# Performance work log

Measured on AMD Instinct MI355X. Metric: run time of the kernel, lower is better.

The kernel has to match this reference:

```python
import jax, jax.numpy as jnp
import numpy as np

B, S, D, E, K = 4, 2048, 1024, 8, 2


def setup_inputs() -> dict:
    key = jax.random.key(0)
    k1, k2, k3 = jax.random.split(key, 3)
    scale = 1.0 / np.sqrt(D)
    x = jax.random.normal(k1, (B, S, D), dtype=jnp.float32)
    Wg = jax.random.normal(k2, (D, E), dtype=jnp.float32) * scale
    bg = jnp.zeros((E,), dtype=jnp.float32)
    We = jax.random.normal(k3, (E, D, D), dtype=jnp.float32) * scale
    be = jnp.zeros((E, D), dtype=jnp.float32)
    return {"x": x, "Wg": Wg, "bg": bg, "We": We, "be": be}


def reference(x, Wg, bg, We, be):
    # gate scores: [B, S, E]
    gate_scores = jnp.einsum("bsd,de->bse", x, Wg) + bg
    topk_values, topk_indices = jax.lax.top_k(gate_scores, K)
    # mask: -inf everywhere except at top-k indices (where value == score)
    sel = jax.nn.one_hot(topk_indices, E, dtype=jnp.bool_).any(axis=-2)  # [B,S,E]
    masked = jnp.where(sel, gate_scores, -jnp.inf)
    gate_weights = jax.nn.softmax(masked, axis=-1)  # [B,S,E]
    # dense all-expert compute, as in the original: [B,S,E,D]
    expert_outputs = jnp.einsum("bsd,edh->bseh", x, We) + be
    fused = jnp.einsum("bse,bseh->bsh", gate_weights, expert_outputs)
    return fused
```

## Files before the change

### kernel.cpp

```cpp
#include <hip/hip_runtime.h>
#include <stdint.h>

#define NTOK   8192
#define DIM    1024
#define NEXP   8
#define MAXP   8192

typedef float    f32x4  __attribute__((ext_vector_type(4)));
typedef __bf16   bf16x8 __attribute__((ext_vector_type(8)));
typedef _Float16 h16x8  __attribute__((ext_vector_type(8)));

typedef __attribute__((address_space(1))) const void* gas_ptr;
typedef __attribute__((address_space(3))) void*       las_ptr;

__device__ __forceinline__ unsigned short f32_to_bf16(float f) {
  union { float f; unsigned int u; } v; v.f = f;
  unsigned int u = v.u;
  unsigned int r = (u + 0x7FFFu + ((u >> 16) & 1u)) >> 16;
  return (unsigned short)r;
}

__global__ __launch_bounds__(256) void wprep_kernel(
    const float* __restrict__ We, unsigned short* __restrict__ Wf) {
  __shared__ float tile[64][65];
  const int bid = blockIdx.x;
  const int e  = bid >> 8;
  const int d0 = ((bid >> 4) & 15) * 64;
  const int h0 = (bid & 15) * 64;
  const int t  = threadIdx.x;
  const float* src = We + (size_t)e * DIM * DIM;
  const int rr = t >> 4;
  const int cc = (t & 15) * 4;
#pragma unroll
  for (int p = 0; p < 4; ++p) {
    const int row = rr + p * 16;
    f32x4 v = *(const f32x4*)(src + (size_t)(d0 + row) * DIM + (h0 + cc));
    tile[row][cc]     = v[0];
    tile[row][cc + 1] = v[1];
    tile[row][cc + 2] = v[2];
    tile[row][cc + 3] = v[3];
  }
  __syncthreads();
  const int nt    = h0 >> 7;
  const int rbase = h0 & 64;
  const int hl    = t >> 2;
  const int k8    = t & 3;
#pragma unroll
  for (int reg = 0; reg < 2; ++reg) {
    const int kt = (d0 >> 5) + reg;
    unsigned int pk[4];
#pragma unroll
    for (int q = 0; q < 4; ++q) {
      int dl = reg * 32 + k8 * 8 + q * 2;
      pk[q] = (unsigned int)f32_to_bf16(tile[dl][hl]) |
              ((unsigned int)f32_to_bf16(tile[dl + 1][hl]) << 16);
    }
    size_t base = (((size_t)(e * 8 + nt) * 32 + kt) << 12) +
                  (size_t)(rbase + hl) * 32 + k8 * 8;
    *(uint4*)&Wf[base] = make_uint4(pk[0], pk[1], pk[2], pk[3]);
  }
}

__global__ __launch_bounds__(256) void gate_kernel(
    const float* __restrict__ x, const float* __restrict__ Wg,
    const float* __restrict__ bg, unsigned short* __restrict__ Xbf,
    int* __restrict__ tok_ee, float2* __restrict__ tok_w) {
  const int wave = threadIdx.x >> 6;
  const int lane = threadIdx.x & 63;
  const int tok0 = blockIdx.x * 16 + wave * 4;

  float xs[4][16];
#pragma unroll
  for (int t = 0; t < 4; ++t) {
    const float* xr = x + (size_t)(tok0 + t) * DIM + lane * 16;
#pragma unroll
    for (int i = 0; i < 4; ++i)
      *(f32x4*)&xs[t][i * 4] = *(const f32x4*)(xr + i * 4);
  }
#pragma unroll
  for (int t = 0; t < 4; ++t) {
    unsigned int pk[8];
#pragma unroll
    for (int i = 0; i < 8; ++i)
      pk[i] = (unsigned int)f32_to_bf16(xs[t][2 * i]) |
              ((unsigned int)f32_to_bf16(xs[t][2 * i + 1]) << 16);
    uint4* xb = (uint4*)(Xbf + (size_t)(tok0 + t) * DIM + lane * 16);
    xb[0] = make_uint4(pk[0], pk[1], pk[2], pk[3]);
    xb[1] = make_uint4(pk[4], pk[5], pk[6], pk[7]);
  }

  double acc[4][8];
#pragma unroll
  for (int t = 0; t < 4; ++t)
#pragma unroll
    for (int e = 0; e < 8; ++e) acc[t][e] = 0.0;

  const float* wr = Wg + (size_t)(lane * 16) * NEXP;
#pragma unroll
  for (int i = 0; i < 16; ++i) {
    f32x4 wa = *(const f32x4*)(wr + i * 8);
    f32x4 wb = *(const f32x4*)(wr + i * 8 + 4);
    double w0 = wa[0], w1 = wa[1], w2 = wa[2], w3 = wa[3];
    double w4 = wb[0], w5 = wb[1], w6 = wb[2], w7 = wb[3];
#pragma unroll
    for (int t = 0; t < 4; ++t) {
      double xd = (double)xs[t][i];
      acc[t][0] += xd * w0; acc[t][1] += xd * w1;
      acc[t][2] += xd * w2; acc[t][3] += xd * w3;
      acc[t][4] += xd * w4; acc[t][5] += xd * w5;
      acc[t][6] += xd * w6; acc[t][7] += xd * w7;
    }
  }
#pragma unroll
  for (int m = 1; m < 64; m <<= 1)
#pragma unroll
    for (int t = 0; t < 4; ++t)
#pragma unroll
      for (int e = 0; e < 8; ++e) acc[t][e] += __shfl_xor(acc[t][e], m, 64);

  if (lane == 0) {
#pragma unroll
    for (int t = 0; t < 4; ++t) {
      float s[8];
#pragma unroll
      for (int e = 0; e < 8; ++e) s[e] = (float)acc[t][e] + bg[e];
      int i0 = 0; float v0 = s[0];
#pragma unroll
      for (int e = 1; e < 8; ++e) if (s[e] > v0) { v0 = s[e]; i0 = e; }
      int i1 = -1; float v1 = -3.4e38f;
#pragma unroll
      for (int e = 0; e < 8; ++e) if (e != i0 && s[e] > v1) { v1 = s[e]; i1 = e; }
      float t1 = expf(v1 - v0);
      float den = 1.0f + t1;
      tok_ee[tok0 + t] = i0 | (i1 << 8);
      tok_w[tok0 + t]  = make_float2(1.0f / den, t1 / den);
    }
  }
}

__global__ __launch_bounds__(1024) void compact_kernel(
    const int* __restrict__ tok_ee, const float2* __restrict__ tok_w,
    int* __restrict__ counts, int* __restrict__ pair_token,
    float* __restrict__ pair_w) {
  __shared__ int wave_cnt[16];
  __shared__ int wave_off[16];
  const int e = blockIdx.x;
  const int tid = threadIdx.x, wave = tid >> 6, lane = tid & 63;
  int base = 0;
  for (int c = 0; c < NTOK / 1024; ++c) {
    const int t = c * 1024 + tid;
    const int p = tok_ee[t];
    const bool m0 = ((p & 255) == e);
    const bool m1 = (((p >> 8) & 255) == e);
    const unsigned long long m = __ballot(m0 || m1);
    const int pre = __popcll(m & ((1ull << lane) - 1ull));
    if (lane == 0) wave_cnt[wave] = __popcll(m);
    __syncthreads();
    if (tid == 0) {
      int s = base;
      for (int w = 0; w < 16; ++w) { wave_off[w] = s; s += wave_cnt[w]; }
      base = s;
    }
    __syncthreads();
    if (m0 || m1) {
      const float2 w = tok_w[t];
      const int slot = wave_off[wave] + pre;
      pair_token[e * MAXP + slot] = (t << 1) | (m1 ? 1 : 0);
      pair_w[e * MAXP + slot]     = m1 ? w.y : w.x;
    }
    __syncthreads();
  }
  if (tid == 0) counts[e] = base;
}

__global__ __launch_bounds__(512, 4) void moe_gemm(
    const unsigned short* __restrict__ Xbf, const unsigned short* __restrict__ Wf,
    const float* __restrict__ be, const int* __restrict__ counts,
    const int* __restrict__ pair_token, const float* __restrict__ pair_w,
    _Float16* __restrict__ part, float* __restrict__ Y, int use_part) {
  const int id    = blockIdx.x;
  const int e     = id & 7;
  const int ntile = (id >> 3) & 3;
  const int m0    = (id >> 5) * 128;
  const int cnt   = counts[e];
  if (m0 >= cnt) return;

  __shared__ __align__(16) unsigned short As[3][128 * 32];
  __shared__ __align__(16) unsigned short Bs[3][256 * 32];

  const int tid  = threadIdx.x;
  const int wave = tid >> 6;
  const int lane = tid & 63;
  const int fm   = lane & 15;
  const int fq   = lane >> 4;
  const int wm   = wave >> 2;
  const int wn   = wave & 3;

  const int kc = (((lane & 3) ^ ((lane >> 3) & 3)) * 8);
  const int grA = m0 + wave * 16 + (lane >> 2);
  const int tkA = (grA < cnt) ? (pair_token[e * MAXP + grA] >> 1) : 0;
  const unsigned short* gA = Xbf + (size_t)tkA * DIM + kc;
  const unsigned short* gB[2];
#pragma unroll
  for (int l = 0; l < 2; ++l) {
    const int R16 = wave * 2 + l;
    const int cg  = ntile * 2 + (R16 >> 3);
    gB[l] = Wf + ((size_t)(e * 8 + cg) << 17) +
            (size_t)((R16 & 7) * 16 + (lane >> 2)) * 32 + kc;
  }

#define STAGE(buf, k0v)                                                       \
  {                                                                           \
    __builtin_amdgcn_global_load_lds(                                         \
        (gas_ptr)(uintptr_t)(gA + (k0v)),                                     \
        (las_ptr)(uintptr_t)(&As[buf][wave * 512]), 16, 0, 0);                \
    _Pragma("unroll") for (int l = 0; l < 2; ++l)                             \
      __builtin_amdgcn_global_load_lds(                                       \
          (gas_ptr)(uintptr_t)(gB[l] + (size_t)(k0v) * 128),                  \
          (las_ptr)(uintptr_t)(&Bs[buf][(wave * 2 + l) * 512]), 16, 0, 0);    \
  }

  f32x4 acc[4][4];
#pragma unroll
  for (int i = 0; i < 4; ++i)
#pragma unroll
    for (int j = 0; j < 4; ++j) { f32x4 z = {0.f, 0.f, 0.f, 0.f}; acc[i][j] = z; }

  const int rdo  = (fq ^ ((fm >> 1) & 3)) * 8;
  const int arow = (wm * 64 + fm) * 32 + rdo;
  const int brow = (wn * 64 + fm) * 32 + rdo;

  STAGE(0, 0);
  STAGE(1, 32);
  int cur = 0;
  for (int k0 = 0; k0 < DIM; k0 += 32) {
    asm volatile("s_waitcnt vmcnt(3)" ::: "memory");
    __builtin_amdgcn_s_barrier();

    int kn = k0 + 64;
    if (kn >= DIM) kn = 0;
    int nb = cur + 2;
    if (nb >= 3) nb -= 3;
    STAGE(nb, kn);

    bf16x8 af[4], bfr[4];
#pragma unroll
    for (int i = 0; i < 4; ++i)
      af[i] = *(const bf16x8*)&As[cur][arow + i * 512];
#pragma unroll
    for (int j = 0; j < 4; ++j)
      bfr[j] = *(const bf16x8*)&Bs[cur][brow + j * 512];
#pragma unroll
    for (int i = 0; i < 4; ++i)
#pragma unroll
      for (int j = 0; j < 4; ++j)
        acc[i][j] = __builtin_amdgcn_mfma_f32_16x16x32_bf16(af[i], bfr[j],
                                                            acc[i][j], 0, 0, 0);
    cur = (cur + 1 == 3) ? 0 : cur + 1;
  }
  asm volatile("s_waitcnt vmcnt(0)" ::: "memory");
#undef STAGE

#pragma unroll
  for (int i = 0; i < 4; ++i) {
    int   rv[4];
    float wv[4];
#pragma unroll
    for (int r = 0; r < 4; ++r) {
      int gr = m0 + wm * 64 + i * 16 + fq * 4 + r;
      bool valid = gr < cnt;
      rv[r] = valid ? pair_token[e * MAXP + gr] : -1;
      wv[r] = valid ? pair_w[e * MAXP + gr] : 0.f;
    }
    if (use_part) {
#pragma unroll
      for (int j = 0; j < 4; ++j) {
        int col = ntile * 256 + wn * 64 + j * 16 + fm;
        float bev = be[e * DIM + col];
#pragma unroll
        for (int r = 0; r < 4; ++r) {
          int v = rv[r];
          if (v >= 0)
            __builtin_nontemporal_store(
                (_Float16)(wv[r] * (acc[i][j][r] + bev)),
                &part[(size_t)v * DIM + col]);
        }
      }
    } else {
#pragma unroll
      for (int j = 0; j < 4; ++j) {
        int col = ntile * 256 + wn * 64 + j * 16 + fm;
        float bev = be[e * DIM + col];
#pragma unroll
        for (int r = 0; r < 4; ++r) {
          int v = rv[r];
          if (v >= 0)
            atomicAdd(Y + (size_t)(v >> 1) * DIM + col,
                      wv[r] * (acc[i][j][r] + bev));
        }
      }
    }
  }
}

__global__ __launch_bounds__(256) void reduce_pairs(
    const _Float16* __restrict__ part, float* __restrict__ Y) {
  const int g = blockIdx.x * 256 + threadIdx.x;
  const int t = g >> 7;
  const int o = (g & 127) * 8;
  const h16x8 a =
      __builtin_nontemporal_load((const h16x8*)(part + (size_t)(2 * t) * DIM + o));
  const h16x8 b =
      __builtin_nontemporal_load((const h16x8*)(part + (size_t)(2 * t + 1) * DIM + o));
  float* y = Y + (size_t)t * DIM + o;
  f32x4 lo = {(float)a[0] + (float)b[0], (float)a[1] + (float)b[1],
              (float)a[2] + (float)b[2], (float)a[3] + (float)b[3]};
  f32x4 hi = {(float)a[4] + (float)b[4], (float)a[5] + (float)b[5],
              (float)a[6] + (float)b[6], (float)a[7] + (float)b[7]};
  __builtin_nontemporal_store(lo, (f32x4*)y);
  __builtin_nontemporal_store(hi, (f32x4*)(y + 4));
}

extern "C" void kernel_launch(void* const* d_in, const int* in_sizes, int n_in,
                              void* d_out, int out_size, void* d_ws, size_t ws_size,
                              hipStream_t stream) {
  const float* x  = (const float*)d_in[0];
  const float* Wg = (const float*)d_in[1];
  const float* bg = (const float*)d_in[2];
  const float* We = (const float*)d_in[3];
  const float* be = (const float*)d_in[4];
  float* Y = (float*)d_out;

  const size_t MB = 1024 * 1024;
  char* ws = (char*)d_ws;
  unsigned short* Xbf = (unsigned short*)ws;
  unsigned short* Wf  = (unsigned short*)(ws + 16 * MB);
  const size_t part_bytes = (size_t)NTOK * 2 * DIM * 2;
  const size_t need = 32 * MB + part_bytes + 1 * MB;
  const int use_part = ws_size >= need;
  _Float16* part = (_Float16*)(ws + 32 * MB);
  char* p2 = ws + 32 * MB + (use_part ? part_bytes : 0);
  int*    counts     = (int*)p2;
  int*    pair_token = (int*)(p2 + 256);
  float*  pair_w     = (float*)(p2 + 256 + 262144);
  int*    tok_ee     = (int*)(p2 + 256 + 2 * 262144);
  float2* tok_w      = (float2*)(p2 + 256 + 2 * 262144 + 32768);

  if (!use_part)
    hipMemsetAsync(d_out, 0, (size_t)out_size * sizeof(float), stream);

  wprep_kernel<<<2048, 256, 0, stream>>>(We, Wf);
  gate_kernel<<<512, 256, 0, stream>>>(x, Wg, bg, Xbf, tok_ee, tok_w);
  compact_kernel<<<NEXP, 1024, 0, stream>>>(tok_ee, tok_w, counts, pair_token,
                                            pair_w);
  moe_gemm<<<8 * 4 * (MAXP / 128), 512, 0, stream>>>(
      Xbf, Wf, be, counts, pair_token, pair_w, part, Y, use_part);
  if (use_part)
    reduce_pairs<<<NTOK * DIM / 8 / 256, 256, 0, stream>>>(part, Y);
}
```

Before: 219.2 us.

## Pre-gather routed token rows into tiled contiguous A buffer before MoE GEMM

Adds a gather kernel that copies each expert's routed bf16 token rows into a k-tiled, contiguous layout (Ap) matching the GEMM's LDS tile format. The GEMM then streams A tiles with contiguous loads instead of indirect per-row gathers from Xbf, for the first 4096 slots per expert. This removes scattered row reads from the GEMM's inner loop but adds an extra kernel launch and a 64 MB write plus re-read of workspace. The new path only runs if the workspace is large enough.

```diff
diff --git a/kernel.cpp b/kernel.cpp
--- a/kernel.cpp
+++ b/kernel.cpp
@@ -6,9 +6,10 @@
 #define NEXP   8
 #define MAXP   8192
 
-typedef float    f32x4  __attribute__((ext_vector_type(4)));
-typedef __bf16   bf16x8 __attribute__((ext_vector_type(8)));
-typedef _Float16 h16x8  __attribute__((ext_vector_type(8)));
+typedef float        f32x4  __attribute__((ext_vector_type(4)));
+typedef unsigned int u32x4  __attribute__((ext_vector_type(4)));
+typedef __bf16       bf16x8 __attribute__((ext_vector_type(8)));
+typedef _Float16     h16x8  __attribute__((ext_vector_type(8)));
 
 typedef __attribute__((address_space(1))) const void* gas_ptr;
 typedef __attribute__((address_space(3))) void*       las_ptr;
@@ -57,7 +58,8 @@
     }
     size_t base = (((size_t)(e * 8 + nt) * 32 + kt) << 12) +
                   (size_t)(rbase + hl) * 32 + k8 * 8;
-    *(uint4*)&Wf[base] = make_uint4(pk[0], pk[1], pk[2], pk[3]);
+    u32x4 w = {pk[0], pk[1], pk[2], pk[3]};
+    *(u32x4*)&Wf[base] = w;
   }
 }
 
@@ -84,9 +86,11 @@
     for (int i = 0; i < 8; ++i)
       pk[i] = (unsigned int)f32_to_bf16(xs[t][2 * i]) |
               ((unsigned int)f32_to_bf16(xs[t][2 * i + 1]) << 16);
-    uint4* xb = (uint4*)(Xbf + (size_t)(tok0 + t) * DIM + lane * 16);
-    xb[0] = make_uint4(pk[0], pk[1], pk[2], pk[3]);
-    xb[1] = make_uint4(pk[4], pk[5], pk[6], pk[7]);
+    u32x4* xb = (u32x4*)(Xbf + (size_t)(tok0 + t) * DIM + lane * 16);
+    u32x4 w0 = {pk[0], pk[1], pk[2], pk[3]};
+    u32x4 w1 = {pk[4], pk[5], pk[6], pk[7]};
+    xb[0] = w0;
+    xb[1] = w1;
   }
 
   double acc[4][8];
@@ -173,11 +177,51 @@
   if (tid == 0) counts[e] = base;
 }
 
+__global__ __launch_bounds__(256) void gather_kernel(
+    const unsigned short* __restrict__ Xbf, const int* __restrict__ counts,
+    const int* __restrict__ pair_token, unsigned short* __restrict__ Ap) {
+  __shared__ __align__(16) unsigned short rows[16][1040];
+  const int bid = blockIdx.x;
+  const int e  = bid & 7;
+  const int g  = (bid >> 3) & 7;
+  const int mt = bid >> 6;
+  const int cnt = counts[e];
+  const int m0g = mt * 128 + g * 16;
+  if (m0g >= ((cnt + 127) & ~127)) return;
+  const int wave = threadIdx.x >> 6, lane = threadIdx.x & 63;
+#pragma unroll
+  for (int q = 0; q < 4; ++q) {
+    const int r    = wave * 4 + q;
+    const int slot = m0g + r;
+    u32x4 v0 = {0u, 0u, 0u, 0u}, v1 = {0u, 0u, 0u, 0u};
+    if (slot < cnt) {
+      const int tok = pair_token[e * MAXP + slot] >> 1;
+      const u32x4* src = (const u32x4*)(Xbf + (size_t)tok * DIM + lane * 8);
+      v0 = src[0];
+      v1 = src[64];
+    }
+    *(u32x4*)&rows[r][lane * 8]       = v0;
+    *(u32x4*)&rows[r][lane * 8 + 512] = v1;
+  }
+  __syncthreads();
+  const int r  = lane >> 2;
+  const int k8 = lane & 3;
+  unsigned short* dst0 = Ap + (((size_t)(e * 32 + mt) * 32) << 12) +
+                         (size_t)(g * 16 + r) * 32 + k8 * 8;
+#pragma unroll
+  for (int q = 0; q < 8; ++q) {
+    const int kt = wave * 8 + q;
+    u32x4 v = *(const u32x4*)&rows[r][kt * 32 + k8 * 8];
+    __builtin_nontemporal_store(v, (u32x4*)(dst0 + ((size_t)kt << 12)));
+  }
+}
+
 __global__ __launch_bounds__(512, 4) void moe_gemm(
     const unsigned short* __restrict__ Xbf, const unsigned short* __restrict__ Wf,
-    const float* __restrict__ be, const int* __restrict__ counts,
-    const int* __restrict__ pair_token, const float* __restrict__ pair_w,
-    _Float16* __restrict__ part, float* __restrict__ Y, int use_part) {
+    const unsigned short* __restrict__ Ap, const float* __restrict__ be,
+    const int* __restrict__ counts, const int* __restrict__ pair_token,
+    const float* __restrict__ pair_w, _Float16* __restrict__ part,
+    float* __restrict__ Y, int use_part, int use_ap) {
   const int id    = blockIdx.x;
   const int e     = id & 7;
   const int ntile = (id >> 3) & 3;
@@ -197,9 +241,18 @@
   const int wn   = wave & 3;
 
   const int kc = (((lane & 3) ^ ((lane >> 3) & 3)) * 8);
-  const int grA = m0 + wave * 16 + (lane >> 2);
-  const int tkA = (grA < cnt) ? (pair_token[e * MAXP + grA] >> 1) : 0;
-  const unsigned short* gA = Xbf + (size_t)tkA * DIM + kc;
+  const unsigned short* gA;
+  size_t astep;
+  if (use_ap && m0 < 4096) {
+    gA = Ap + (((size_t)(e * 32 + (m0 >> 7)) * 32) << 12) +
+         (size_t)(wave * 16 + (lane >> 2)) * 32 + kc;
+    astep = 128;
+  } else {
+    const int grA = m0 + wave * 16 + (lane >> 2);
+    const int tkA = (grA < cnt) ? (pair_token[e * MAXP + grA] >> 1) : 0;
+    gA = Xbf + (size_t)tkA * DIM + kc;
+    astep = 1;
+  }
   const unsigned short* gB[2];
 #pragma unroll
   for (int l = 0; l < 2; ++l) {
@@ -212,7 +265,7 @@
 #define STAGE(buf, k0v)                                                       \
   {                                                                           \
     __builtin_amdgcn_global_load_lds(                                         \
-        (gas_ptr)(uintptr_t)(gA + (k0v)),                                     \
+        (gas_ptr)(uintptr_t)(gA + (size_t)(k0v) * astep),                     \
         (las_ptr)(uintptr_t)(&As[buf][wave * 512]), 16, 0, 0);                \
     _Pragma("unroll") for (int l = 0; l < 2; ++l)                             \
       __builtin_amdgcn_global_load_lds(                                       \
@@ -336,10 +389,22 @@
   unsigned short* Xbf = (unsigned short*)ws;
   unsigned short* Wf  = (unsigned short*)(ws + 16 * MB);
   const size_t part_bytes = (size_t)NTOK * 2 * DIM * 2;
-  const size_t need = 32 * MB + part_bytes + 1 * MB;
-  const int use_part = ws_size >= need;
-  _Float16* part = (_Float16*)(ws + 32 * MB);
-  char* p2 = ws + 32 * MB + (use_part ? part_bytes : 0);
+  const size_t need_old = 32 * MB + part_bytes + 1 * MB;
+  const size_t ap_bytes = (size_t)8 * 32 * 32 * 4096 * 2;
+  const size_t need_ap  = 32 * MB + ap_bytes + part_bytes + 1 * MB;
+  const int use_ap   = ws_size >= need_ap;
+  const int use_part = ws_size >= need_old;
+
+  unsigned short* Aprime = (unsigned short*)(ws + 32 * MB);
+  _Float16* part;
+  char* p2;
+  if (use_ap) {
+    part = (_Float16*)(ws + 96 * MB);
+    p2   = ws + 96 * MB + part_bytes;
+  } else {
+    part = (_Float16*)(ws + 32 * MB);
+    p2   = ws + 32 * MB + (use_part ? part_bytes : 0);
+  }
   int*    counts     = (int*)p2;
   int*    pair_token = (int*)(p2 + 256);
   float*  pair_w     = (float*)(p2 + 256 + 262144);
@@ -347,14 +412,17 @@
   float2* tok_w      = (float2*)(p2 + 256 + 2 * 262144 + 32768);
 
   if (!use_part)
-    hipMemsetAsync(d_out, 0, (size_t)out_size * sizeof(float), stream);
+    (void)hipMemsetAsync(d_out, 0, (size_t)out_size * sizeof(float), stream);
 
   wprep_kernel<<<2048, 256, 0, stream>>>(We, Wf);
   gate_kernel<<<512, 256, 0, stream>>>(x, Wg, bg, Xbf, tok_ee, tok_w);
   compact_kernel<<<NEXP, 1024, 0, stream>>>(tok_ee, tok_w, counts, pair_token,
                                             pair_w);
+  if (use_ap)
+    gather_kernel<<<2048, 256, 0, stream>>>(Xbf, counts, pair_token, Aprime);
   moe_gemm<<<8 * 4 * (MAXP / 128), 512, 0, stream>>>(
-      Xbf, Wf, be, counts, pair_token, pair_w, part, Y, use_part);
+      Xbf, Wf, Aprime, be, counts, pair_token, pair_w, part, Y, use_part,
+      use_ap);
   if (use_part)
     reduce_pairs<<<NTOK * DIM / 8 / 256, 256, 0, stream>>>(part, Y);
 }
```

Result: slower. 245.7 us (+12.1%).

## Enlarge MoE GEMM M-tile to 160 rows with persistent grid-stride loop

Applied to the files above, without the earlier changes.

The MoE grouped GEMM tile grows from 128 to 160 rows (5 MFMA row blocks per wave, with two waves loading the extra A rows). The grid becomes a fixed 512 blocks that stride over M tiles, replacing the launch of one block per possible tile and the early exits for empty tiles. This raises arithmetic intensity per B-tile load and removes idle blocks. In exchange it uses more accumulator registers and LDS, and the waves issue uneven load counts, which changes the wait counts.

```diff
diff --git a/kernel.cpp b/kernel.cpp
--- a/kernel.cpp
+++ b/kernel.cpp
@@ -6,9 +6,10 @@
 #define NEXP   8
 #define MAXP   8192
 
-typedef float    f32x4  __attribute__((ext_vector_type(4)));
-typedef __bf16   bf16x8 __attribute__((ext_vector_type(8)));
-typedef _Float16 h16x8  __attribute__((ext_vector_type(8)));
+typedef float        f32x4  __attribute__((ext_vector_type(4)));
+typedef unsigned int u32x4  __attribute__((ext_vector_type(4)));
+typedef __bf16       bf16x8 __attribute__((ext_vector_type(8)));
+typedef _Float16     h16x8  __attribute__((ext_vector_type(8)));
 
 typedef __attribute__((address_space(1))) const void* gas_ptr;
 typedef __attribute__((address_space(3))) void*       las_ptr;
@@ -57,7 +58,8 @@
     }
     size_t base = (((size_t)(e * 8 + nt) * 32 + kt) << 12) +
                   (size_t)(rbase + hl) * 32 + k8 * 8;
-    *(uint4*)&Wf[base] = make_uint4(pk[0], pk[1], pk[2], pk[3]);
+    u32x4 w = {pk[0], pk[1], pk[2], pk[3]};
+    *(u32x4*)&Wf[base] = w;
   }
 }
 
@@ -84,9 +86,11 @@
     for (int i = 0; i < 8; ++i)
       pk[i] = (unsigned int)f32_to_bf16(xs[t][2 * i]) |
               ((unsigned int)f32_to_bf16(xs[t][2 * i + 1]) << 16);
-    uint4* xb = (uint4*)(Xbf + (size_t)(tok0 + t) * DIM + lane * 16);
-    xb[0] = make_uint4(pk[0], pk[1], pk[2], pk[3]);
-    xb[1] = make_uint4(pk[4], pk[5], pk[6], pk[7]);
+    u32x4* xb = (u32x4*)(Xbf + (size_t)(tok0 + t) * DIM + lane * 16);
+    u32x4 w0 = {pk[0], pk[1], pk[2], pk[3]};
+    u32x4 w1 = {pk[4], pk[5], pk[6], pk[7]};
+    xb[0] = w0;
+    xb[1] = w1;
   }
 
   double acc[4][8];
@@ -181,11 +185,10 @@
   const int id    = blockIdx.x;
   const int e     = id & 7;
   const int ntile = (id >> 3) & 3;
-  const int m0    = (id >> 5) * 128;
+  const int mt    = id >> 5;
   const int cnt   = counts[e];
-  if (m0 >= cnt) return;
-
-  __shared__ __align__(16) unsigned short As[3][128 * 32];
+
+  __shared__ __align__(16) unsigned short As[3][160 * 32];
   __shared__ __align__(16) unsigned short Bs[3][256 * 32];
 
   const int tid  = threadIdx.x;
@@ -197,9 +200,6 @@
   const int wn   = wave & 3;
 
   const int kc = (((lane & 3) ^ ((lane >> 3) & 3)) * 8);
-  const int grA = m0 + wave * 16 + (lane >> 2);
-  const int tkA = (grA < cnt) ? (pair_token[e * MAXP + grA] >> 1) : 0;
-  const unsigned short* gA = Xbf + (size_t)tkA * DIM + kc;
   const unsigned short* gB[2];
 #pragma unroll
   for (int l = 0; l < 2; ++l) {
@@ -209,94 +209,109 @@
             (size_t)((R16 & 7) * 16 + (lane >> 2)) * 32 + kc;
   }
 
+  const int rdo  = (fq ^ ((fm >> 1) & 3)) * 8;
+  const int arow = (wm * 80 + fm) * 32 + rdo;
+  const int brow = (wn * 64 + fm) * 32 + rdo;
+
+  for (int m0 = mt * 160; m0 < cnt; m0 += 2560) {
+    __syncthreads();
+
+    const int grA0 = m0 + wave * 16 + (lane >> 2);
+    const int tk0  = (grA0 < cnt) ? (pair_token[e * MAXP + grA0] >> 1) : 0;
+    const unsigned short* gA0 = Xbf + (size_t)tk0 * DIM + kc;
+    const int grA1 = m0 + 128 + wave * 16 + (lane >> 2);
+    const int tk1  = (grA1 < cnt) ? (pair_token[e * MAXP + grA1] >> 1) : 0;
+    const unsigned short* gA1 = Xbf + (size_t)tk1 * DIM + kc;
+
 #define STAGE(buf, k0v)                                                       \
   {                                                                           \
     __builtin_amdgcn_global_load_lds(                                         \
-        (gas_ptr)(uintptr_t)(gA + (k0v)),                                     \
+        (gas_ptr)(uintptr_t)(gA0 + (k0v)),                                    \
         (las_ptr)(uintptr_t)(&As[buf][wave * 512]), 16, 0, 0);                \
+    if (wave < 2)                                                             \
+      __builtin_amdgcn_global_load_lds(                                       \
+          (gas_ptr)(uintptr_t)(gA1 + (k0v)),                                  \
+          (las_ptr)(uintptr_t)(&As[buf][(8 + wave) * 512]), 16, 0, 0);        \
     _Pragma("unroll") for (int l = 0; l < 2; ++l)                             \
       __builtin_amdgcn_global_load_lds(                                       \
           (gas_ptr)(uintptr_t)(gB[l] + (size_t)(k0v) * 128),                  \
           (las_ptr)(uintptr_t)(&Bs[buf][(wave * 2 + l) * 512]), 16, 0, 0);    \
   }
 
-  f32x4 acc[4][4];
-#pragma unroll
-  for (int i = 0; i < 4; ++i)
-#pragma unroll
-    for (int j = 0; j < 4; ++j) { f32x4 z = {0.f, 0.f, 0.f, 0.f}; acc[i][j] = z; }
-
-  const int rdo  = (fq ^ ((fm >> 1) & 3)) * 8;
-  const int arow = (wm * 64 + fm) * 32 + rdo;
-  const int brow = (wn * 64 + fm) * 32 + rdo;
-
-  STAGE(0, 0);
-  STAGE(1, 32);
-  int cur = 0;
-  for (int k0 = 0; k0 < DIM; k0 += 32) {
-    asm volatile("s_waitcnt vmcnt(3)" ::: "memory");
-    __builtin_amdgcn_s_barrier();
-
-    int kn = k0 + 64;
-    if (kn >= DIM) kn = 0;
-    int nb = cur + 2;
-    if (nb >= 3) nb -= 3;
-    STAGE(nb, kn);
-
-    bf16x8 af[4], bfr[4];
-#pragma unroll
-    for (int i = 0; i < 4; ++i)
-      af[i] = *(const bf16x8*)&As[cur][arow + i * 512];
-#pragma unroll
-    for (int j = 0; j < 4; ++j)
-      bfr[j] = *(const bf16x8*)&Bs[cur][brow + j * 512];
-#pragma unroll
-    for (int i = 0; i < 4; ++i)
+    f32x4 acc[5][4];
+#pragma unroll
+    for (int i = 0; i < 5; ++i)
+#pragma unroll
+      for (int j = 0; j < 4; ++j) { f32x4 z = {0.f, 0.f, 0.f, 0.f}; acc[i][j] = z; }
+
+    STAGE(0, 0);
+    STAGE(1, 32);
+    int cur = 0;
+    for (int k0 = 0; k0 < DIM; k0 += 32) {
+      if (wave < 2) { asm volatile("s_waitcnt vmcnt(4)" ::: "memory"); }
+      else          { asm volatile("s_waitcnt vmcnt(3)" ::: "memory"); }
+      __builtin_amdgcn_s_barrier();
+
+      int kn = k0 + 64;
+      if (kn >= DIM) kn = 0;
+      int nb = cur + 2;
+      if (nb >= 3) nb -= 3;
+      STAGE(nb, kn);
+
+      bf16x8 bfr[4];
 #pragma unroll
       for (int j = 0; j < 4; ++j)
-        acc[i][j] = __builtin_amdgcn_mfma_f32_16x16x32_bf16(af[i], bfr[j],
-                                                            acc[i][j], 0, 0, 0);
-    cur = (cur + 1 == 3) ? 0 : cur + 1;
-  }
-  asm volatile("s_waitcnt vmcnt(0)" ::: "memory");
+        bfr[j] = *(const bf16x8*)&Bs[cur][brow + j * 512];
+#pragma unroll
+      for (int i = 0; i < 5; ++i) {
+        bf16x8 af = *(const bf16x8*)&As[cur][arow + i * 512];
+#pragma unroll
+        for (int j = 0; j < 4; ++j)
+          acc[i][j] = __builtin_amdgcn_mfma_f32_16x16x32_bf16(af, bfr[j],
+                                                              acc[i][j], 0, 0, 0);
+      }
+      cur = (cur + 1 == 3) ? 0 : cur + 1;
+    }
+    asm volatile("s_waitcnt vmcnt(0)" ::: "memory");
 #undef STAGE
 
 #pragma unroll
-  for (int i = 0; i < 4; ++i) {
-    int   rv[4];
-    float wv[4];
-#pragma unroll
-    for (int r = 0; r < 4; ++r) {
-      int gr = m0 + wm * 64 + i * 16 + fq * 4 + r;
-      bool valid = gr < cnt;
-      rv[r] = valid ? pair_token[e * MAXP + gr] : -1;
-      wv[r] = valid ? pair_w[e * MAXP + gr] : 0.f;
-    }
-    if (use_part) {
-#pragma unroll
-      for (int j = 0; j < 4; ++j) {
-        int col = ntile * 256 + wn * 64 + j * 16 + fm;
-        float bev = be[e * DIM + col];
-#pragma unroll
-        for (int r = 0; r < 4; ++r) {
-          int v = rv[r];
-          if (v >= 0)
-            __builtin_nontemporal_store(
-                (_Float16)(wv[r] * (acc[i][j][r] + bev)),
-                &part[(size_t)v * DIM + col]);
+    for (int i = 0; i < 5; ++i) {
+      int   rv[4];
+      float wv[4];
+#pragma unroll
+      for (int r = 0; r < 4; ++r) {
+        int gr = m0 + wm * 80 + i * 16 + fq * 4 + r;
+        bool valid = gr < cnt;
+        rv[r] = valid ? pair_token[e * MAXP + gr] : -1;
+        wv[r] = valid ? pair_w[e * MAXP + gr] : 0.f;
+      }
+      if (use_part) {
+#pragma unroll
+        for (int j = 0; j < 4; ++j) {
+          int col = ntile * 256 + wn * 64 + j * 16 + fm;
+          float bev = be[e * DIM + col];
+#pragma unroll
+          for (int r = 0; r < 4; ++r) {
+            int v = rv[r];
+            if (v >= 0)
+              __builtin_nontemporal_store(
+                  (_Float16)(wv[r] * (acc[i][j][r] + bev)),
+                  &part[(size_t)v * DIM + col]);
+          }
         }
-      }
-    } else {
-#pragma unroll
-      for (int j = 0; j < 4; ++j) {
-        int col = ntile * 256 + wn * 64 + j * 16 + fm;
-        float bev = be[e * DIM + col];
-#pragma unroll
-        for (int r = 0; r < 4; ++r) {
-          int v = rv[r];
-          if (v >= 0)
-            atomicAdd(Y + (size_t)(v >> 1) * DIM + col,
-                      wv[r] * (acc[i][j][r] + bev));
+      } else {
+#pragma unroll
+        for (int j = 0; j < 4; ++j) {
+          int col = ntile * 256 + wn * 64 + j * 16 + fm;
+          float bev = be[e * DIM + col];
+#pragma unroll
+          for (int r = 0; r < 4; ++r) {
+            int v = rv[r];
+            if (v >= 0)
+              atomicAdd(Y + (size_t)(v >> 1) * DIM + col,
+                        wv[r] * (acc[i][j][r] + bev));
+          }
         }
       }
     }
@@ -347,13 +362,13 @@
   float2* tok_w      = (float2*)(p2 + 256 + 2 * 262144 + 32768);
 
   if (!use_part)
-    hipMemsetAsync(d_out, 0, (size_t)out_size * sizeof(float), stream);
+    (void)hipMemsetAsync(d_out, 0, (size_t)out_size * sizeof(float), stream);
 
   wprep_kernel<<<2048, 256, 0, stream>>>(We, Wf);
   gate_kernel<<<512, 256, 0, stream>>>(x, Wg, bg, Xbf, tok_ee, tok_w);
   compact_kernel<<<NEXP, 1024, 0, stream>>>(tok_ee, tok_w, counts, pair_token,
                                             pair_w);
-  moe_gemm<<<8 * 4 * (MAXP / 128), 512, 0, stream>>>(
+  moe_gemm<<<8 * 4 * 16, 512, 0, stream>>>(
       Xbf, Wf, be, counts, pair_token, pair_w, part, Y, use_part);
   if (use_part)
     reduce_pairs<<<NTOK * DIM / 8 / 256, 256, 0, stream>>>(part, Y);
```

New measurement: 209.2 us. 1.05x faster.
